# Performance work log

Measured on AMD Instinct MI355X. Metric: run time of the kernel, lower is better.

Reference implementation:

```python
import jax, jax.numpy as jnp
import numpy as np

B, S, L, H, D, DF = 2, 1024, 2, 8, 512, 2048
DK = D // H  # head dim (dk == dv == 64)
EPS = 1e-5


def _ln(x, g, b):
    m = jnp.mean(x, axis=-1, keepdims=True)
    v = jnp.mean((x - m) ** 2, axis=-1, keepdims=True)
    return (x - m) / jnp.sqrt(v + EPS) * g + b


def setup_inputs() -> dict:
    key = jax.random.key(0)
    ks = jax.random.split(key, 8)
    sd = 1.0 / np.sqrt(D)
    sf = 1.0 / np.sqrt(DF)
    inp = {
        "src": jax.random.normal(ks[0], (B, S, D), jnp.float32),
        "Wq": jax.random.normal(ks[1], (L, D, D), jnp.float32) * sd,
        "bq": jnp.zeros((L, D), jnp.float32),
        "Wk": jax.random.normal(ks[2], (L, D, D), jnp.float32) * sd,
        "bk": jnp.zeros((L, D), jnp.float32),
        "Wv": jax.random.normal(ks[3], (L, D, D), jnp.float32) * sd,
        "bv": jnp.zeros((L, D), jnp.float32),
        "Wo": jax.random.normal(ks[4], (L, D, D), jnp.float32) * sd,
        "bo": jnp.zeros((L, D), jnp.float32),
        "W1": jax.random.normal(ks[5], (L, D, DF), jnp.float32) * sd,
        "b1": jnp.zeros((L, DF), jnp.float32),
        "W2": jax.random.normal(ks[6], (L, DF, D), jnp.float32) * sf,
        "b2": jnp.zeros((L, D), jnp.float32),
        "g1": jnp.ones((L, D), jnp.float32),
        "be1": jnp.zeros((L, D), jnp.float32),
        "g2": jnp.ones((L, D), jnp.float32),
        "be2": jnp.zeros((L, D), jnp.float32),
        "gf": jnp.ones((D,), jnp.float32),
        "bef": jnp.zeros((D,), jnp.float32),
    }
    return inp


def _heads(x):
    # [B,S,D] -> [B,H,S,DK]
    return x.reshape(B, S, H, DK).transpose(0, 2, 1, 3)


def _causal_linear_attention(q, k, v):
    # Faithful to torch: cumsum of per-step KV outer products, then query contraction.
    kv = jnp.einsum("bhsk,bhsv->bhskv", k, v)      # [B,H,S,DK,DK]
    cum = jnp.cumsum(kv, axis=2)                     # prefix sums over sequence
    return jnp.einsum("bhsk,bhskv->bhsv", q, cum)   # [B,H,S,DK]


def reference(src, Wq, bq, Wk, bk, Wv, bv, Wo, bo, W1, b1, W2, b2,
              g1, be1, g2, be2, gf, bef):
    x = src
    for i in range(L):
        q = _heads(x @ Wq[i] + bq[i])
        k = _heads(x @ Wk[i] + bk[i])
        v = _heads(x @ Wv[i] + bv[i])
        att = _causal_linear_attention(q, k, v)
        att = att.transpose(0, 2, 1, 3).reshape(B, S, D)
        att = att @ Wo[i] + bo[i]
        x = _ln(x + att, g1[i], be1[i])              # post-norm (normalize_before=False)
        ff = jax.nn.relu(x @ W1[i] + b1[i]) @ W2[i] + b2[i]
        x = _ln(x + ff, g2[i], be2[i])
    return _ln(x, gf, bef)                            # final encoder LayerNorm
```

## Files before the change

kernel.cpp:

```cpp
#include <hip/hip_runtime.h>
#include <hip/hip_bf16.h>

#define DEV static __device__ __forceinline__

typedef __attribute__((ext_vector_type(8))) short short8;
typedef __attribute__((ext_vector_type(4))) float f32x4;

DEV unsigned short f2b(float f){
  unsigned int u = __float_as_uint(f);
  return (unsigned short)((u + 0x7FFFu + ((u >> 16) & 1u)) >> 16);
}
DEV float b2f(unsigned short h){ return __uint_as_float(((unsigned int)h) << 16); }
DEV float load_in(const void* p, size_t i, int isbf){
  return isbf ? b2f(((const unsigned short*)p)[i]) : ((const float*)p)[i];
}
DEV void load_lds16(const unsigned short* g, unsigned short* l){
  __builtin_amdgcn_global_load_lds(
      (const __attribute__((address_space(1))) void*)g,
      (__attribute__((address_space(3))) void*)l, 16, 0, 0);
}

DEV int detect_isbf_block(const void* src){
  __shared__ int cnt[4];
  int tid = threadIdx.x;
  float v = b2f(((const unsigned short*)src)[2 * tid]);
  float av = fabsf(v);
  bool sane = ((av < 64.0f) && (av > 9.5e-7f)) || (v == 0.0f);
  unsigned long long m = __ballot(sane);
  if ((tid & 63) == 0) cnt[tid >> 6] = __popcll(m);
  __syncthreads();
  int tot = cnt[0] + cnt[1] + cnt[2] + cnt[3];
  __syncthreads();
  return tot > 128;
}

struct WDesc { const void* src; long src_off; unsigned short* dst; int K; int N; int tstart; };
struct WParams { WDesc d[12]; const void* dsrc; };

__global__ __launch_bounds__(256) void ingest_weights(WParams P){
  __shared__ float tile[32][33];
  int isbf = detect_isbf_block(P.dsrc);
  int b = blockIdx.x;
  int t = 0;
  #pragma unroll
  for (int i = 1; i < 12; ++i) if (b >= P.d[i].tstart) t = i;
  WDesc d = P.d[t];
  int r = b - d.tstart;
  int tiles_x = d.N >> 5;
  int tx = r % tiles_x, ty = r / tiles_x;
  int lx = threadIdx.x & 31, ly = threadIdx.x >> 5;
  #pragma unroll
  for (int i = 0; i < 4; ++i){
    int row = ty*32 + ly + i*8;
    int col = tx*32 + lx;
    tile[ly + i*8][lx] = load_in(d.src, (size_t)d.src_off + (size_t)row*d.N + col, isbf);
  }
  __syncthreads();
  #pragma unroll
  for (int i = 0; i < 4; ++i){
    int orow = tx*32 + ly + i*8;
    int ocol = ty*32 + lx;
    d.dst[(size_t)orow*d.K + ocol] = f2b(tile[lx][ly + i*8]);
  }
}

struct SDesc { const void* src; int src_off; int dstart; };
struct SParams { SDesc d[22]; float* dst; int total; };

__global__ __launch_bounds__(256) void ingest_misc(SParams S, const void* src,
                                                   float* xf, unsigned short* xb){
  int isbf = detect_isbf_block(src);
  int b = blockIdx.x, tid = threadIdx.x;
  if (b < 4096){
    int i = b*256 + tid;
    float v = load_in(src, (size_t)i, isbf);
    xf[i] = v; xb[i] = f2b(v);
  } else {
    int i = (b - 4096)*256 + tid;
    if (i < S.total){
      int t = 0;
      #pragma unroll
      for (int j = 1; j < 22; ++j) if (i >= S.d[j].dstart) t = j;
      S.dst[i] = load_in(S.d[t].src, (size_t)S.d[t].src_off + (i - S.d[t].dstart), isbf);
    }
  }
}

struct GemmArgs {
  const unsigned short* A;
  const unsigned short* Bt;
  const float* bias;
  float* Cf;
  unsigned short* Cb;
  int K;
  int lda, ldb, ldc;
  int cshift, cmask;
  size_t cstride;
  size_t cfz;
  int relu;
};

template<int BN>
__global__ __launch_bounds__(256) void gemm_bt(GemmArgs g){
  constexpr int NI = (BN == 128) ? 4 : 2;
  constexpr int NJ = 4;
  __shared__ __align__(16) unsigned short sA[128*32];
  __shared__ __align__(16) unsigned short sB[BN*32];
  int tid = threadIdx.x;
  int koff = blockIdx.z * g.K;
  int K = g.K, lda = g.lda, ldb = g.ldb;
  size_t bm = (size_t)blockIdx.y * 128, bn = (size_t)blockIdx.x * BN;
  int lane = tid & 63, wv = tid >> 6, quad = lane >> 4, l16 = lane & 15;
  int wm = (BN == 128) ? (wv >> 1) * 64 : wv * 32;
  int wn = (BN == 128) ? (wv & 1) * 64 : 0;
  f32x4 acc[NI][NJ];
  #pragma unroll
  for (int i=0;i<NI;++i)
    #pragma unroll
    for (int j=0;j<NJ;++j) acc[i][j] = (f32x4){0.f,0.f,0.f,0.f};
  const unsigned short* Ap = g.A  + (bm + (tid>>2))*lda + koff + (tid&3)*8;
  const unsigned short* Bp = g.Bt + (bn + (tid>>2))*ldb + koff + (tid&3)*8;
  for (int ko = 0; ko < K; ko += 32){
    __syncthreads();
    load_lds16(Ap + ko,                  &sA[tid*8]);
    load_lds16(Ap + (size_t)64*lda + ko, &sA[2048 + tid*8]);
    load_lds16(Bp + ko,                  &sB[tid*8]);
    if (BN == 128)
      load_lds16(Bp + (size_t)64*ldb + ko, &sB[2048 + tid*8]);
    __syncthreads();
    short8 af[NI], bfv[NJ];
    #pragma unroll
    for (int i=0;i<NI;++i) af[i]  = *(const short8*)&sA[(wm + i*16 + l16)*32 + quad*8];
    #pragma unroll
    for (int j=0;j<NJ;++j) bfv[j] = *(const short8*)&sB[(wn + j*16 + l16)*32 + quad*8];
    #pragma unroll
    for (int i=0;i<NI;++i)
      #pragma unroll
      for (int j=0;j<NJ;++j)
        acc[i][j] = __builtin_amdgcn_mfma_f32_16x16x32_bf16(af[i], bfv[j], acc[i][j], 0,0,0);
  }
  float* Cf = g.Cf ? g.Cf + (size_t)blockIdx.z * g.cfz : nullptr;
  unsigned short* Cb = g.Cb;
  #pragma unroll
  for (int j=0;j<NJ;++j){
    int col = (int)bn + wn + j*16 + l16;
    float bv = g.bias ? g.bias[col] : 0.f;
    size_t cbase = ((size_t)(col >> g.cshift))*g.cstride + (col & g.cmask);
    #pragma unroll
    for (int i=0;i<NI;++i){
      #pragma unroll
      for (int r=0;r<4;++r){
        int row = (int)bm + wm + i*16 + quad*4 + r;
        float v = acc[i][j][r] + bv;
        if (g.relu) v = fmaxf(v, 0.f);
        size_t idx = cbase + (size_t)row*g.ldc;
        if (Cf) Cf[idx] = v;
        if (Cb) Cb[idx] = f2b(v);
      }
    }
  }
}

#define ATT_S 1024
#define ATT_D 512

__global__ __launch_bounds__(256) void attn_state_kernel(
    const unsigned short* k, const unsigned short* v, float* states)
{
  __shared__ __align__(16) unsigned short sVt[64*72];
  __shared__ __align__(16) unsigned short sKt[64*72];
  int tid = threadIdx.x;
  int c = blockIdx.x, bh = blockIdx.y;
  int b = bh >> 3, h = bh & 7;
  const size_t base = ((size_t)b*ATT_S + (size_t)c*64)*ATT_D + h*64;
  int lane = tid & 63, wv = tid >> 6, quad = lane >> 4, l16 = lane & 15;

  int t = lane, vc = wv*8;
  const unsigned short* vp = v + base + (size_t)t*ATT_D;
  const unsigned short* kp = k + base + (size_t)t*ATT_D;
  float4 v0 = *(const float4*)(vp + vc);
  float4 v1 = *(const float4*)(vp + vc + 32);
  float4 k0 = *(const float4*)(kp + vc);
  float4 k1 = *(const float4*)(kp + vc + 32);
  {
    const unsigned short* pv0 = (const unsigned short*)&v0;
    const unsigned short* pv1 = (const unsigned short*)&v1;
    const unsigned short* pk0 = (const unsigned short*)&k0;
    const unsigned short* pk1 = (const unsigned short*)&k1;
    #pragma unroll
    for (int e = 0; e < 8; ++e){
      sVt[(vc+e)*72 + t]    = pv0[e];
      sVt[(vc+32+e)*72 + t] = pv1[e];
      sKt[(vc+e)*72 + t]    = pk0[e];
      sKt[(vc+32+e)*72 + t] = pk1[e];
    }
  }
  __syncthreads();

  f32x4 acc[4];
  #pragma unroll
  for (int j=0;j<4;++j) acc[j] = (f32x4){0.f,0.f,0.f,0.f};
  #pragma unroll
  for (int kk=0;kk<2;++kk){
    short8 a = *(const short8*)&sVt[(wv*16 + l16)*72 + kk*32 + quad*8];
    #pragma unroll
    for (int j=0;j<4;++j){
      short8 bb = *(const short8*)&sKt[(j*16 + l16)*72 + kk*32 + quad*8];
      acc[j] = __builtin_amdgcn_mfma_f32_16x16x32_bf16(a, bb, acc[j], 0,0,0);
    }
  }
  float* st = states + ((size_t)bh*16 + c)*4096;
  #pragma unroll
  for (int j=0;j<4;++j)
    #pragma unroll
    for (int rr=0;rr<4;++rr)
      st[(wv*16 + quad*4 + rr)*64 + j*16 + l16] = acc[j][rr];
}

__global__ __launch_bounds__(256) void attn_out_kernel(
    const unsigned short* q, const unsigned short* k, const unsigned short* v,
    const float* states, unsigned short* att)
{
  __shared__ __align__(16) unsigned short sQ [64*72];
  __shared__ __align__(16) unsigned short sK [64*72];
  __shared__ __align__(16) unsigned short sVt[64*72];
  __shared__ __align__(16) float sKV[64*68];
  int tid = threadIdx.x;
  int c = blockIdx.x, bh = blockIdx.y;
  int b = bh >> 3, h = bh & 7;
  const size_t base = ((size_t)b*ATT_S + (size_t)c*64)*ATT_D + h*64;
  int lane = tid & 63, wv = tid >> 6, quad = lane >> 4, l16 = lane & 15;

  float4 racc[4];
  #pragma unroll
  for (int u=0;u<4;++u) racc[u] = (float4){0.f,0.f,0.f,0.f};
  const float* sbase = states + (size_t)bh*16*4096;
  for (int cc = 0; cc < c; ++cc){
    const float4* sp = (const float4*)(sbase + (size_t)cc*4096);
    #pragma unroll
    for (int u=0;u<4;++u){
      float4 t4 = sp[tid + u*256];
      racc[u].x += t4.x; racc[u].y += t4.y; racc[u].z += t4.z; racc[u].w += t4.w;
    }
  }
  #pragma unroll
  for (int u=0;u<4;++u){
    int e = (tid + u*256)*4;
    int row = e >> 6, col = e & 63;
    *(float4*)&sKV[row*68 + col] = racc[u];
  }

  int r = tid >> 2, c8 = (tid & 3)*8;
  const unsigned short* qp = q + base + (size_t)r*ATT_D;
  const unsigned short* kp = k + base + (size_t)r*ATT_D;
  float4 q0 = *(const float4*)(qp + c8);
  float4 q1 = *(const float4*)(qp + c8 + 32);
  float4 k0 = *(const float4*)(kp + c8);
  float4 k1 = *(const float4*)(kp + c8 + 32);
  int t = lane, vc = wv*8;
  const unsigned short* vp = v + base + (size_t)t*ATT_D;
  float4 v0 = *(const float4*)(vp + vc);
  float4 v1 = *(const float4*)(vp + vc + 32);
  *(float4*)&sQ[r*72 + c8]      = q0;
  *(float4*)&sQ[r*72 + c8 + 32] = q1;
  *(float4*)&sK[r*72 + c8]      = k0;
  *(float4*)&sK[r*72 + c8 + 32] = k1;
  {
    const unsigned short* pv0 = (const unsigned short*)&v0;
    const unsigned short* pv1 = (const unsigned short*)&v1;
    #pragma unroll
    for (int e=0;e<8;++e){
      sVt[(vc+e)*72 + t]    = pv0[e];
      sVt[(vc+32+e)*72 + t] = pv1[e];
    }
  }
  __syncthreads();

  f32x4 accS[4];
  #pragma unroll
  for (int j=0;j<4;++j) accS[j] = (f32x4){0.f,0.f,0.f,0.f};
  #pragma unroll
  for (int kk=0;kk<2;++kk){
    short8 a = *(const short8*)&sQ[(wv*16 + l16)*72 + kk*32 + quad*8];
    #pragma unroll
    for (int j=0;j<4;++j){
      short8 bb = *(const short8*)&sK[(j*16 + l16)*72 + kk*32 + quad*8];
      accS[j] = __builtin_amdgcn_mfma_f32_16x16x32_bf16(a, bb, accS[j], 0,0,0);
    }
  }
  __syncthreads();

  #pragma unroll
  for (int j=0;j<4;++j)
    #pragma unroll
    for (int rr=0;rr<4;++rr){
      int i  = wv*16 + quad*4 + rr;
      int cj = j*16 + l16;
      sK[i*72 + cj] = f2b((i >= cj) ? accS[j][rr] : 0.f);
    }

  f32x4 accO[4];
  #pragma unroll
  for (int j=0;j<4;++j) accO[j] = (f32x4){0.f,0.f,0.f,0.f};
  #pragma unroll
  for (int kk=0;kk<2;++kk){
    short8 a = *(const short8*)&sQ[(wv*16 + l16)*72 + kk*32 + quad*8];
    #pragma unroll
    for (int j=0;j<4;++j){
      const float* pf = &sKV[(j*16 + l16)*68 + kk*32 + quad*8];
      short8 bb;
      #pragma unroll
      for (int e=0;e<8;++e) ((unsigned short*)&bb)[e] = f2b(pf[e]);
      accO[j] = __builtin_amdgcn_mfma_f32_16x16x32_bf16(a, bb, accO[j], 0,0,0);
    }
  }
  __syncthreads();

  #pragma unroll
  for (int kk=0;kk<2;++kk){
    short8 a = *(const short8*)&sK[(wv*16 + l16)*72 + kk*32 + quad*8];
    #pragma unroll
    for (int j=0;j<4;++j){
      short8 bb = *(const short8*)&sVt[(j*16 + l16)*72 + kk*32 + quad*8];
      accO[j] = __builtin_amdgcn_mfma_f32_16x16x32_bf16(a, bb, accO[j], 0,0,0);
    }
  }
  #pragma unroll
  for (int j=0;j<4;++j)
    #pragma unroll
    for (int rr=0;rr<4;++rr){
      int i  = wv*16 + quad*4 + rr;
      int cj = j*16 + l16;
      att[base + (size_t)i*ATT_D + cj] = f2b(accO[j][rr]);
    }
}

__global__ __launch_bounds__(256) void add_ln_kernel(
    const float* x, const float* p, int np, const float* bias,
    const float* g, const float* bta,
    float* outf, unsigned short* outb, void* outd, const void* dsrc, int rows)
{
  int isbf = 0;
  if (dsrc) isbf = detect_isbf_block(dsrc);
  int row = blockIdx.x*4 + (threadIdx.x >> 6);
  int lane = threadIdx.x & 63;
  if (row >= rows) return;
  const float* xr = x + (size_t)row*512;
  float a[8];
  *(float4*)&a[0] = *(const float4*)(xr + lane*4);
  *(float4*)&a[4] = *(const float4*)(xr + 256 + lane*4);
  for (int s = 0; s < np; ++s){
    const float* pr = p + (size_t)s*1048576 + (size_t)row*512;
    float yb[8];
    *(float4*)&yb[0] = *(const float4*)(pr + lane*4);
    *(float4*)&yb[4] = *(const float4*)(pr + 256 + lane*4);
    #pragma unroll
    for (int e=0;e<8;++e) a[e] += yb[e];
  }
  if (bias){
    float bb2[8];
    *(float4*)&bb2[0] = *(const float4*)(bias + lane*4);
    *(float4*)&bb2[4] = *(const float4*)(bias + 256 + lane*4);
    #pragma unroll
    for (int e=0;e<8;++e) a[e] += bb2[e];
  }
  float s = 0.f, qq = 0.f;
  #pragma unroll
  for (int e=0;e<8;++e){ s += a[e]; qq += a[e]*a[e]; }
  #pragma unroll
  for (int off=32; off>0; off>>=1){
    s  += __shfl_xor(s,  off, 64);
    qq += __shfl_xor(qq, off, 64);
  }
  float mean = s * (1.f/512.f);
  float var  = qq * (1.f/512.f) - mean*mean;
  float rstd = rsqrtf(var + 1e-5f);
  float gg[8], bb[8];
  *(float4*)&gg[0] = *(const float4*)(g + lane*4);
  *(float4*)&gg[4] = *(const float4*)(g + 256 + lane*4);
  *(float4*)&bb[0] = *(const float4*)(bta + lane*4);
  *(float4*)&bb[4] = *(const float4*)(bta + 256 + lane*4);
  #pragma unroll
  for (int e=0;e<8;++e) a[e] = (a[e]-mean)*rstd*gg[e] + bb[e];
  if (outf){
    float* orow = outf + (size_t)row*512;
    *(float4*)(orow + lane*4)       = *(float4*)&a[0];
    *(float4*)(orow + 256 + lane*4) = *(float4*)&a[4];
  }
  if (outb){
    unsigned short* orow = outb + (size_t)row*512;
    #pragma unroll
    for (int e=0;e<4;++e){ orow[lane*4+e] = f2b(a[e]); orow[256+lane*4+e] = f2b(a[4+e]); }
  }
  if (outd){
    if (isbf){
      unsigned short* od = (unsigned short*)outd + (size_t)row*512;
      #pragma unroll
      for (int e=0;e<4;++e){ od[lane*4+e] = f2b(a[e]); od[256+lane*4+e] = f2b(a[4+e]); }
    } else {
      float* od = (float*)outd + (size_t)row*512;
      *(float4*)(od + lane*4)       = *(float4*)&a[0];
      *(float4*)(od + 256 + lane*4) = *(float4*)&a[4];
    }
  }
}

extern "C" void kernel_launch(void* const* d_in, const int* in_sizes, int n_in,
                              void* d_out, int out_size, void* d_ws, size_t ws_size,
                              hipStream_t stream)
{
  (void)in_sizes; (void)n_in; (void)out_size; (void)ws_size;
  const void* src = d_in[0];
  const void* Wq = d_in[1];  const void* bq = d_in[2];
  const void* Wk = d_in[3];  const void* bk = d_in[4];
  const void* Wv = d_in[5];  const void* bv = d_in[6];
  const void* Wo = d_in[7];  const void* bo = d_in[8];
  const void* W1 = d_in[9];  const void* b1 = d_in[10];
  const void* W2 = d_in[11]; const void* b2 = d_in[12];
  const void* g1 = d_in[13]; const void* be1 = d_in[14];
  const void* g2 = d_in[15]; const void* be2 = d_in[16];
  const void* gf = d_in[17]; const void* bef = d_in[18];

  char* W = (char*)d_ws;
  float* smalls          = (float*)(W + 256);
  unsigned short* wt     = (unsigned short*)(W + 65536);
  float* x_f             = (float*)(W + 12648448);
  unsigned short* x_b    = (unsigned short*)(W + 16842752);
  unsigned short* q_b    = (unsigned short*)(W + 18939904);
  unsigned short* att_b  = (unsigned short*)(W + 25231360);
  float* pp              = (float*)(W + 27328512);
  unsigned short* h1_b   = (unsigned short*)(W + 44105728);
  float* states          = (float*)(W + 44105728);
  unsigned short* k_b = q_b + 1048576;
  unsigned short* v_b = q_b + 2097152;

  WParams wp;
  {
    const void* wsrc[6] = {Wq, Wk, Wv, Wo, W1, W2};
    int wK[6] = {512,512,512,512,512,2048};
    int wN[6] = {512,512,512,512,2048,512};
    long wsz[6] = {262144,262144,262144,262144,1048576,1048576};
    int tstart = 0; size_t dsto = 0;
    for (int l=0;l<2;++l)
      for (int ti=0;ti<6;++ti){
        int idx = l*6+ti;
        wp.d[idx].src = wsrc[ti];
        wp.d[idx].src_off = (long)l * wsz[ti];
        wp.d[idx].dst = wt + dsto;
        wp.d[idx].K = wK[ti]; wp.d[idx].N = wN[ti];
        wp.d[idx].tstart = tstart;
        tstart += (wK[ti]/32)*(wN[ti]/32);
        dsto += (size_t)wsz[ti];
      }
    wp.dsrc = src;
    ingest_weights<<<dim3(6144), 256, 0, stream>>>(wp);
  }

  SParams sp;
  {
    const void* ss[10] = {bq,bk,bv,bo,b1,b2,g1,be1,g2,be2};
    int slen[10] = {512,512,512,512,2048,512,512,512,512,512};
    int dcur = 0, di = 0;
    for (int l=0;l<2;++l)
      for (int ti=0;ti<10;++ti){
        sp.d[di].src = ss[ti];
        sp.d[di].src_off = l * slen[ti];
        sp.d[di].dstart = dcur;
        dcur += slen[ti]; ++di;
      }
    sp.d[20].src = gf;  sp.d[20].src_off = 0; sp.d[20].dstart = dcur; dcur += 512;
    sp.d[21].src = bef; sp.d[21].src_off = 0; sp.d[21].dstart = dcur; dcur += 512;
    sp.dst = smalls; sp.total = dcur;
    ingest_misc<<<dim3(4152), 256, 0, stream>>>(sp, src, x_f, x_b);
  }

  for (int l = 0; l < 2; ++l){
    unsigned short* WqkvT = wt + (size_t)l*3145728;
    unsigned short* WoT   = WqkvT + 786432;
    unsigned short* W1T   = WqkvT + 1048576;
    unsigned short* W2T   = WqkvT + 2097152;
    float* base  = smalls + l*6656;
    float* p_bqkv= base;
    float* p_bo  = base + 1536;
    float* p_b1  = base + 2048;
    float* p_b2  = base + 4096;
    float* p_g1  = base + 4608;
    float* p_be1 = base + 5120;
    float* p_g2  = base + 5632;
    float* p_be2 = base + 6144;

    GemmArgs qkv = {};
    qkv.A = x_b; qkv.Bt = WqkvT; qkv.bias = p_bqkv;
    qkv.Cf = nullptr; qkv.Cb = q_b;
    qkv.K = 512; qkv.lda = 512; qkv.ldb = 512; qkv.ldc = 512;
    qkv.cshift = 9; qkv.cmask = 511; qkv.cstride = 1048576; qkv.cfz = 0; qkv.relu = 0;
    gemm_bt<64><<<dim3(24,16,1), 256, 0, stream>>>(qkv);

    attn_state_kernel<<<dim3(16,16), 256, 0, stream>>>(k_b, v_b, states);
    attn_out_kernel<<<dim3(16,16), 256, 0, stream>>>(q_b, k_b, v_b, states, att_b);

    GemmArgs go = {};
    go.A = att_b; go.Bt = WoT; go.bias = nullptr;
    go.Cf = pp; go.Cb = nullptr;
    go.K = 256; go.lda = 512; go.ldb = 512; go.ldc = 512;
    go.cshift = 30; go.cmask = 0x3fffffff; go.cstride = 0; go.cfz = 1048576; go.relu = 0;
    gemm_bt<64><<<dim3(8,16,2), 256, 0, stream>>>(go);

    add_ln_kernel<<<dim3(512), 256, 0, stream>>>(x_f, pp, 2, p_bo, p_g1, p_be1,
                                                 x_f, x_b, nullptr, nullptr, 2048);

    GemmArgs f1 = {};
    f1.A = x_b; f1.Bt = W1T; f1.bias = p_b1;
    f1.Cf = nullptr; f1.Cb = h1_b;
    f1.K = 512; f1.lda = 512; f1.ldb = 512; f1.ldc = 2048;
    f1.cshift = 30; f1.cmask = 0x3fffffff; f1.cstride = 0; f1.cfz = 0; f1.relu = 1;
    gemm_bt<128><<<dim3(16,16,1), 256, 0, stream>>>(f1);

    GemmArgs f2 = {};
    f2.A = h1_b; f2.Bt = W2T; f2.bias = nullptr;
    f2.Cf = pp; f2.Cb = nullptr;
    f2.K = 512; f2.lda = 2048; f2.ldb = 2048; f2.ldc = 512;
    f2.cshift = 30; f2.cmask = 0x3fffffff; f2.cstride = 0; f2.cfz = 1048576; f2.relu = 0;
    gemm_bt<64><<<dim3(8,16,4), 256, 0, stream>>>(f2);

    add_ln_kernel<<<dim3(512), 256, 0, stream>>>(x_f, pp, 4, p_b2, p_g2, p_be2,
                                                 x_f, x_b, nullptr, nullptr, 2048);
  }

  add_ln_kernel<<<dim3(512), 256, 0, stream>>>(x_f, nullptr, 0, nullptr,
                                               smalls + 13312, smalls + 13824,
                                               nullptr, nullptr, d_out, src, 2048);
}
```

Measured before the change: 280.8 us.

## Fuse ingest kernels and compute attention prefix state in-block

Merges the weight-transpose and misc/input ingest kernels into a single launch. Removes the separate attention state kernel and its fp32 state buffer. Each attention block instead recomputes the K^T V sums of all preceding chunks with MFMA directly from bf16 K/V. This cuts two launches and the global state write/read, at the cost of redundant quadratic recomputation: later chunks loop over up to 15 previous chunks, each with extra syncthreads, which causes load imbalance across blocks.

```diff
diff --git a/kernel.cpp b/kernel.cpp
--- a/kernel.cpp
+++ b/kernel.cpp
@@ -35,53 +35,52 @@
 }
 
 struct WDesc { const void* src; long src_off; unsigned short* dst; int K; int N; int tstart; };
-struct WParams { WDesc d[12]; const void* dsrc; };
-
-__global__ __launch_bounds__(256) void ingest_weights(WParams P){
+struct SDesc { const void* src; int src_off; int dstart; };
+struct IngestParams {
+  WDesc wd[12];
+  SDesc sd[22];
+  float* sdst; int stotal;
+  const void* src;
+  float* xf; unsigned short* xb;
+};
+
+__global__ __launch_bounds__(256) void ingest_all(IngestParams P){
   __shared__ float tile[32][33];
-  int isbf = detect_isbf_block(P.dsrc);
-  int b = blockIdx.x;
-  int t = 0;
-  #pragma unroll
-  for (int i = 1; i < 12; ++i) if (b >= P.d[i].tstart) t = i;
-  WDesc d = P.d[t];
-  int r = b - d.tstart;
-  int tiles_x = d.N >> 5;
-  int tx = r % tiles_x, ty = r / tiles_x;
-  int lx = threadIdx.x & 31, ly = threadIdx.x >> 5;
-  #pragma unroll
-  for (int i = 0; i < 4; ++i){
-    int row = ty*32 + ly + i*8;
-    int col = tx*32 + lx;
-    tile[ly + i*8][lx] = load_in(d.src, (size_t)d.src_off + (size_t)row*d.N + col, isbf);
-  }
-  __syncthreads();
-  #pragma unroll
-  for (int i = 0; i < 4; ++i){
-    int orow = tx*32 + ly + i*8;
-    int ocol = ty*32 + lx;
-    d.dst[(size_t)orow*d.K + ocol] = f2b(tile[lx][ly + i*8]);
-  }
-}
-
-struct SDesc { const void* src; int src_off; int dstart; };
-struct SParams { SDesc d[22]; float* dst; int total; };
-
-__global__ __launch_bounds__(256) void ingest_misc(SParams S, const void* src,
-                                                   float* xf, unsigned short* xb){
-  int isbf = detect_isbf_block(src);
+  int isbf = detect_isbf_block(P.src);
   int b = blockIdx.x, tid = threadIdx.x;
-  if (b < 4096){
-    int i = b*256 + tid;
-    float v = load_in(src, (size_t)i, isbf);
-    xf[i] = v; xb[i] = f2b(v);
+  if (b < 6144){
+    int t = 0;
+    #pragma unroll
+    for (int i = 1; i < 12; ++i) if (b >= P.wd[i].tstart) t = i;
+    WDesc d = P.wd[t];
+    int r = b - d.tstart;
+    int tiles_x = d.N >> 5;
+    int tx = r % tiles_x, ty = r / tiles_x;
+    int lx = tid & 31, ly = tid >> 5;
+    #pragma unroll
+    for (int i = 0; i < 4; ++i){
+      int row = ty*32 + ly + i*8;
+      int col = tx*32 + lx;
+      tile[ly + i*8][lx] = load_in(d.src, (size_t)d.src_off + (size_t)row*d.N + col, isbf);
+    }
+    __syncthreads();
+    #pragma unroll
+    for (int i = 0; i < 4; ++i){
+      int orow = tx*32 + ly + i*8;
+      int ocol = ty*32 + lx;
+      d.dst[(size_t)orow*d.K + ocol] = f2b(tile[lx][ly + i*8]);
+    }
+  } else if (b < 10240){
+    int i = (b - 6144)*256 + tid;
+    float v = load_in(P.src, (size_t)i, isbf);
+    P.xf[i] = v; P.xb[i] = f2b(v);
   } else {
-    int i = (b - 4096)*256 + tid;
-    if (i < S.total){
+    int i = (b - 10240)*256 + tid;
+    if (i < P.stotal){
       int t = 0;
       #pragma unroll
-      for (int j = 1; j < 22; ++j) if (i >= S.d[j].dstart) t = j;
-      S.dst[i] = load_in(S.d[t].src, (size_t)S.d[t].src_off + (i - S.d[t].dstart), isbf);
+      for (int j = 1; j < 22; ++j) if (i >= P.sd[j].dstart) t = j;
+      P.sdst[i] = load_in(P.sd[t].src, (size_t)P.sd[t].src_off + (i - P.sd[t].dstart), isbf);
     }
   }
 }
@@ -164,92 +163,65 @@
 #define ATT_S 1024
 #define ATT_D 512
 
-__global__ __launch_bounds__(256) void attn_state_kernel(
-    const unsigned short* k, const unsigned short* v, float* states)
-{
-  __shared__ __align__(16) unsigned short sVt[64*72];
-  __shared__ __align__(16) unsigned short sKt[64*72];
-  int tid = threadIdx.x;
-  int c = blockIdx.x, bh = blockIdx.y;
-  int b = bh >> 3, h = bh & 7;
-  const size_t base = ((size_t)b*ATT_S + (size_t)c*64)*ATT_D + h*64;
-  int lane = tid & 63, wv = tid >> 6, quad = lane >> 4, l16 = lane & 15;
-
-  int t = lane, vc = wv*8;
-  const unsigned short* vp = v + base + (size_t)t*ATT_D;
-  const unsigned short* kp = k + base + (size_t)t*ATT_D;
-  float4 v0 = *(const float4*)(vp + vc);
-  float4 v1 = *(const float4*)(vp + vc + 32);
-  float4 k0 = *(const float4*)(kp + vc);
-  float4 k1 = *(const float4*)(kp + vc + 32);
-  {
-    const unsigned short* pv0 = (const unsigned short*)&v0;
-    const unsigned short* pv1 = (const unsigned short*)&v1;
-    const unsigned short* pk0 = (const unsigned short*)&k0;
-    const unsigned short* pk1 = (const unsigned short*)&k1;
-    #pragma unroll
-    for (int e = 0; e < 8; ++e){
-      sVt[(vc+e)*72 + t]    = pv0[e];
-      sVt[(vc+32+e)*72 + t] = pv1[e];
-      sKt[(vc+e)*72 + t]    = pk0[e];
-      sKt[(vc+32+e)*72 + t] = pk1[e];
-    }
-  }
-  __syncthreads();
-
-  f32x4 acc[4];
-  #pragma unroll
-  for (int j=0;j<4;++j) acc[j] = (f32x4){0.f,0.f,0.f,0.f};
-  #pragma unroll
-  for (int kk=0;kk<2;++kk){
-    short8 a = *(const short8*)&sVt[(wv*16 + l16)*72 + kk*32 + quad*8];
-    #pragma unroll
-    for (int j=0;j<4;++j){
-      short8 bb = *(const short8*)&sKt[(j*16 + l16)*72 + kk*32 + quad*8];
-      acc[j] = __builtin_amdgcn_mfma_f32_16x16x32_bf16(a, bb, acc[j], 0,0,0);
-    }
-  }
-  float* st = states + ((size_t)bh*16 + c)*4096;
-  #pragma unroll
-  for (int j=0;j<4;++j)
-    #pragma unroll
-    for (int rr=0;rr<4;++rr)
-      st[(wv*16 + quad*4 + rr)*64 + j*16 + l16] = acc[j][rr];
-}
-
-__global__ __launch_bounds__(256) void attn_out_kernel(
+__global__ __launch_bounds__(256) void attn_kernel(
     const unsigned short* q, const unsigned short* k, const unsigned short* v,
-    const float* states, unsigned short* att)
+    unsigned short* att)
 {
   __shared__ __align__(16) unsigned short sQ [64*72];
   __shared__ __align__(16) unsigned short sK [64*72];
   __shared__ __align__(16) unsigned short sVt[64*72];
+  __shared__ __align__(16) unsigned short sKt[64*72];
   __shared__ __align__(16) float sKV[64*68];
   int tid = threadIdx.x;
   int c = blockIdx.x, bh = blockIdx.y;
   int b = bh >> 3, h = bh & 7;
-  const size_t base = ((size_t)b*ATT_S + (size_t)c*64)*ATT_D + h*64;
+  const size_t hoff = ((size_t)b*ATT_S)*ATT_D + h*64;
   int lane = tid & 63, wv = tid >> 6, quad = lane >> 4, l16 = lane & 15;
 
-  float4 racc[4];
-  #pragma unroll
-  for (int u=0;u<4;++u) racc[u] = (float4){0.f,0.f,0.f,0.f};
-  const float* sbase = states + (size_t)bh*16*4096;
+  f32x4 accS[4];
+  #pragma unroll
+  for (int j=0;j<4;++j) accS[j] = (f32x4){0.f,0.f,0.f,0.f};
+  int t = lane, vc = wv*8;
   for (int cc = 0; cc < c; ++cc){
-    const float4* sp = (const float4*)(sbase + (size_t)cc*4096);
-    #pragma unroll
-    for (int u=0;u<4;++u){
-      float4 t4 = sp[tid + u*256];
-      racc[u].x += t4.x; racc[u].y += t4.y; racc[u].z += t4.z; racc[u].w += t4.w;
-    }
-  }
-  #pragma unroll
-  for (int u=0;u<4;++u){
-    int e = (tid + u*256)*4;
-    int row = e >> 6, col = e & 63;
-    *(float4*)&sKV[row*68 + col] = racc[u];
-  }
-
+    const size_t bcc = hoff + (size_t)cc*64*ATT_D;
+    const unsigned short* vp = v + bcc + (size_t)t*ATT_D;
+    const unsigned short* kp = k + bcc + (size_t)t*ATT_D;
+    float4 v0 = *(const float4*)(vp + vc);
+    float4 v1 = *(const float4*)(vp + vc + 32);
+    float4 k0 = *(const float4*)(kp + vc);
+    float4 k1 = *(const float4*)(kp + vc + 32);
+    __syncthreads();
+    {
+      const unsigned short* pv0 = (const unsigned short*)&v0;
+      const unsigned short* pv1 = (const unsigned short*)&v1;
+      const unsigned short* pk0 = (const unsigned short*)&k0;
+      const unsigned short* pk1 = (const unsigned short*)&k1;
+      #pragma unroll
+      for (int e = 0; e < 8; ++e){
+        sVt[(vc+e)*72 + t]    = pv0[e];
+        sVt[(vc+32+e)*72 + t] = pv1[e];
+        sKt[(vc+e)*72 + t]    = pk0[e];
+        sKt[(vc+32+e)*72 + t] = pk1[e];
+      }
+    }
+    __syncthreads();
+    #pragma unroll
+    for (int kk=0;kk<2;++kk){
+      short8 a = *(const short8*)&sVt[(wv*16 + l16)*72 + kk*32 + quad*8];
+      #pragma unroll
+      for (int j=0;j<4;++j){
+        short8 bb = *(const short8*)&sKt[(j*16 + l16)*72 + kk*32 + quad*8];
+        accS[j] = __builtin_amdgcn_mfma_f32_16x16x32_bf16(a, bb, accS[j], 0,0,0);
+      }
+    }
+  }
+  #pragma unroll
+  for (int j=0;j<4;++j)
+    #pragma unroll
+    for (int rr=0;rr<4;++rr)
+      sKV[(wv*16 + quad*4 + rr)*68 + j*16 + l16] = accS[j][rr];
+
+  const size_t base = hoff + (size_t)c*64*ATT_D;
   int r = tid >> 2, c8 = (tid & 3)*8;
   const unsigned short* qp = q + base + (size_t)r*ATT_D;
   const unsigned short* kp = k + base + (size_t)r*ATT_D;
@@ -257,10 +229,10 @@
   float4 q1 = *(const float4*)(qp + c8 + 32);
   float4 k0 = *(const float4*)(kp + c8);
   float4 k1 = *(const float4*)(kp + c8 + 32);
-  int t = lane, vc = wv*8;
   const unsigned short* vp = v + base + (size_t)t*ATT_D;
   float4 v0 = *(const float4*)(vp + vc);
   float4 v1 = *(const float4*)(vp + vc + 32);
+  __syncthreads();
   *(float4*)&sQ[r*72 + c8]      = q0;
   *(float4*)&sQ[r*72 + c8 + 32] = q1;
   *(float4*)&sK[r*72 + c8]      = k0;
@@ -276,16 +248,16 @@
   }
   __syncthreads();
 
-  f32x4 accS[4];
-  #pragma unroll
-  for (int j=0;j<4;++j) accS[j] = (f32x4){0.f,0.f,0.f,0.f};
+  f32x4 accQ[4];
+  #pragma unroll
+  for (int j=0;j<4;++j) accQ[j] = (f32x4){0.f,0.f,0.f,0.f};
   #pragma unroll
   for (int kk=0;kk<2;++kk){
     short8 a = *(const short8*)&sQ[(wv*16 + l16)*72 + kk*32 + quad*8];
     #pragma unroll
     for (int j=0;j<4;++j){
       short8 bb = *(const short8*)&sK[(j*16 + l16)*72 + kk*32 + quad*8];
-      accS[j] = __builtin_amdgcn_mfma_f32_16x16x32_bf16(a, bb, accS[j], 0,0,0);
+      accQ[j] = __builtin_amdgcn_mfma_f32_16x16x32_bf16(a, bb, accQ[j], 0,0,0);
     }
   }
   __syncthreads();
@@ -296,7 +268,7 @@
     for (int rr=0;rr<4;++rr){
       int i  = wv*16 + quad*4 + rr;
       int cj = j*16 + l16;
-      sK[i*72 + cj] = f2b((i >= cj) ? accS[j][rr] : 0.f);
+      sK[i*72 + cj] = f2b((i >= cj) ? accQ[j][rr] : 0.f);
     }
 
   f32x4 accO[4];
@@ -430,11 +402,10 @@
   unsigned short* att_b  = (unsigned short*)(W + 25231360);
   float* pp              = (float*)(W + 27328512);
   unsigned short* h1_b   = (unsigned short*)(W + 44105728);
-  float* states          = (float*)(W + 44105728);
   unsigned short* k_b = q_b + 1048576;
   unsigned short* v_b = q_b + 2097152;
 
-  WParams wp;
+  IngestParams ip;
   {
     const void* wsrc[6] = {Wq, Wk, Wv, Wo, W1, W2};
     int wK[6] = {512,512,512,512,512,2048};
@@ -444,34 +415,29 @@
     for (int l=0;l<2;++l)
       for (int ti=0;ti<6;++ti){
         int idx = l*6+ti;
-        wp.d[idx].src = wsrc[ti];
-        wp.d[idx].src_off = (long)l * wsz[ti];
-        wp.d[idx].dst = wt + dsto;
-        wp.d[idx].K = wK[ti]; wp.d[idx].N = wN[ti];
-        wp.d[idx].tstart = tstart;
+        ip.wd[idx].src = wsrc[ti];
+        ip.wd[idx].src_off = (long)l * wsz[ti];
+        ip.wd[idx].dst = wt + dsto;
+        ip.wd[idx].K = wK[ti]; ip.wd[idx].N = wN[ti];
+        ip.wd[idx].tstart = tstart;
         tstart += (wK[ti]/32)*(wN[ti]/32);
         dsto += (size_t)wsz[ti];
       }
-    wp.dsrc = src;
-    ingest_weights<<<dim3(6144), 256, 0, stream>>>(wp);
-  }
-
-  SParams sp;
-  {
     const void* ss[10] = {bq,bk,bv,bo,b1,b2,g1,be1,g2,be2};
     int slen[10] = {512,512,512,512,2048,512,512,512,512,512};
     int dcur = 0, di = 0;
     for (int l=0;l<2;++l)
       for (int ti=0;ti<10;++ti){
-        sp.d[di].src = ss[ti];
-        sp.d[di].src_off = l * slen[ti];
-        sp.d[di].dstart = dcur;
+        ip.sd[di].src = ss[ti];
+        ip.sd[di].src_off = l * slen[ti];
+        ip.sd[di].dstart = dcur;
         dcur += slen[ti]; ++di;
       }
-    sp.d[20].src = gf;  sp.d[20].src_off = 0; sp.d[20].dstart = dcur; dcur += 512;
-    sp.d[21].src = bef; sp.d[21].src_off = 0; sp.d[21].dstart = dcur; dcur += 512;
-    sp.dst = smalls; sp.total = dcur;
-    ingest_misc<<<dim3(4152), 256, 0, stream>>>(sp, src, x_f, x_b);
+    ip.sd[20].src = gf;  ip.sd[20].src_off = 0; ip.sd[20].dstart = dcur; dcur += 512;
+    ip.sd[21].src = bef; ip.sd[21].src_off = 0; ip.sd[21].dstart = dcur; dcur += 512;
+    ip.sdst = smalls; ip.stotal = dcur;
+    ip.src = src; ip.xf = x_f; ip.xb = x_b;
+    ingest_all<<<dim3(10296), 256, 0, stream>>>(ip);
   }
 
   for (int l = 0; l < 2; ++l){
@@ -496,8 +462,7 @@
     qkv.cshift = 9; qkv.cmask = 511; qkv.cstride = 1048576; qkv.cfz = 0; qkv.relu = 0;
     gemm_bt<64><<<dim3(24,16,1), 256, 0, stream>>>(qkv);
 
-    attn_state_kernel<<<dim3(16,16), 256, 0, stream>>>(k_b, v_b, states);
-    attn_out_kernel<<<dim3(16,16), 256, 0, stream>>>(q_b, k_b, v_b, states, att_b);
+    attn_kernel<<<dim3(16,16), 256, 0, stream>>>(q_b, k_b, v_b, att_b);
 
     GemmArgs go = {};
     go.A = att_b; go.Bt = WoT; go.bias = nullptr;
```

After: 289.7 us. 1.03x slower.
